# Performance work log

Hardware: AMD Instinct MI355X
Metric: run time of the kernel (lower is better)

Reference implementation:

```python
import jax, jax.numpy as jnp
import numpy as np

NUM_ITER = 3  # num_itterations

def squash(s):
    # Faithful to the module's (non-standard) squash: out = |s|^2 * s / (1 + |s|^2 * (|s| + 1e-9)).
    # torch sums over dim=-2 of [..., D, 1]; here s is [..., D] so sum over last axis.
    sq = jnp.sum(s * s, axis=-1, keepdims=True)
    norm = jnp.sqrt(sq)
    return sq * s / (1.0 + sq * (norm + 1e-9))

def setup_inputs() -> dict:
    key = jax.random.key(0)
    k1, k2 = jax.random.split(key)
    B, P, N, T, D = 512, 1152, 10, 16, 8
    x = jax.random.normal(k1, (B, P, D), dtype=jnp.float32)          # input capsules
    W = jax.random.normal(k2, (P, N, T, D), dtype=jnp.float32)       # routing transform (torch W with leading 1 dropped)
    return {"x": x, "W": W}

def reference(x, B_unused=None, *, _=None, **__):
    raise RuntimeError('placeholder')

def reference(x, W):
    # prediction u_hat[b,p,n,:] = W[p,n] @ x[b,p]  -> [B, P, N, T]
    pred = jnp.einsum('pntd,bpd->bpnt', W, x)
    B, P, N = pred.shape[0], pred.shape[1], pred.shape[2]
    b_ij = jnp.zeros((B, P, N), dtype=x.dtype)
    v = None
    for i in range(NUM_ITER):
        # torch.tensor(c_ij) detaches the coupling coefficients from the graph
        c = jax.lax.stop_gradient(jax.nn.softmax(b_ij, axis=2))      # softmax over next-caps dim
        s = jnp.einsum('bpn,bpnt->bnt', c, pred)                     # weighted sum over prev caps
        v = squash(s)                                                # [B, N, T]
        if i < NUM_ITER - 1:
            a = jnp.einsum('bpnt,bnt->bpn', pred, v)                 # agreement
            b_ij = b_ij + jnp.mean(a, axis=0, keepdims=True)         # torch mean over batch, keepdim, broadcast-add
    return v[..., None]  # [B, numNextCaps, nextCapsDim, 1] matching torch v_j.squeeze(1)
```

## Files before the change

kernel.cpp:

```cpp
#include <hip/hip_runtime.h>
#include <hip/hip_bf16.h>


typedef __attribute__((ext_vector_type(8))) short bfrag;
typedef __attribute__((ext_vector_type(4))) float f32x4;

constexpr int B_ = 512, P_ = 1152, N_ = 10, NT_ = 160;
constexpr int K1_ = 9216, NKC_ = 288;

__device__ __forceinline__ unsigned short f2bf(float f) {
    unsigned u = __float_as_uint(f);
    return (unsigned short)((u + 0x7fffu + ((u >> 16) & 1u)) >> 16);
}
__device__ __forceinline__ float bf2f(unsigned short s) {
    return __uint_as_float((unsigned)s << 16);
}
__device__ __forceinline__ bfrag mkfrag(f32x4 a, f32x4 b, float c) {
    bfrag f;
    f[0] = (short)f2bf(a.x * c); f[1] = (short)f2bf(a.y * c);
    f[2] = (short)f2bf(a.z * c); f[3] = (short)f2bf(a.w * c);
    f[4] = (short)f2bf(b.x * c); f[5] = (short)f2bf(b.y * c);
    f[6] = (short)f2bf(b.z * c); f[7] = (short)f2bf(b.w * c);
    return f;
}

__global__ __launch_bounds__(256) void k_prep(const float* __restrict__ x,
                                              const float* __restrict__ W,
                                              unsigned short* __restrict__ Xb,
                                              unsigned short* __restrict__ Xga,
                                              unsigned short* __restrict__ Wc,
                                              unsigned short* __restrict__ Wb) {
    __shared__ float smem[5760];
    const int bid = blockIdx.x, tid = threadIdx.x;
    const int w = tid >> 6, ln = tid & 63, col = ln & 15, q = ln >> 4;
    if (bid < 288) {
        const int pb = bid;
        const int p0 = pb * 4;
#pragma unroll
        for (int k = 0; k < 20; ++k) {
            const int e = k * 256 + tid;
            const int pl = e / 1280, rem = e % 1280;
            const int row = rem >> 3, d = rem & 7;
            smem[pl * 1440 + row * 9 + d] = W[(size_t)p0 * 1280 + e];
        }
        __syncthreads();
        for (int n = w; n < N_; n += 4) {
            const float* src = smem + q * 1440 + (n * 16 + col) * 9;
            bfrag f;
#pragma unroll
            for (int j = 0; j < 8; ++j) f[j] = (short)f2bf(src[j] * 0.1f);
            *(bfrag*)(Wc + ((size_t)(n * NKC_ + pb)) * 512 + ln * 8) = f;
        }
        if (tid < 128) {
            const int pdblk_l = tid >> 6;
            const int lane = tid & 63, c2 = lane & 15, q2 = lane >> 4;
            const int p_l = (pdblk_l * 16 + c2) >> 3, d = c2 & 7;
            const float* src = smem + p_l * 1440 + d;
            unsigned short* dst = Wb + ((size_t)((2 * pb + pdblk_l) * 64 + lane)) * 40;
#pragma unroll
            for (int mt = 0; mt < N_; ++mt)
#pragma unroll
                for (int r = 0; r < 4; ++r)
                    dst[mt * 4 + r] = f2bf(src[(mt * 16 + q2 * 4 + r) * 9]);
        }
    } else {
        unsigned short (*tile)[72] = (unsigned short (*)[72])smem;
        const int tb = bid - 288;
        const int pd0 = (tb >> 3) * 64, b0 = (tb & 7) * 64;
        const int c0 = tid & 63, r0 = tid >> 6;
#pragma unroll
        for (int i = 0; i < 16; ++i) {
            const int br = i * 4 + r0;
            tile[c0][br] = f2bf(x[(size_t)(b0 + br) * K1_ + pd0 + c0]);
        }
        __syncthreads();
#pragma unroll
        for (int fi = 0; fi < 2; ++fi) {
            const int f = w + fi * 4;
            const int pdblk_l = f & 3, kc_l = f >> 2;
            bfrag fr;
#pragma unroll
            for (int j = 0; j < 8; ++j)
                fr[j] = (short)tile[pdblk_l * 16 + col][kc_l * 32 + q * 8 + j];
            const size_t addr = ((size_t)(((pd0 >> 4) + pdblk_l) * 16 + (b0 >> 5) + kc_l)) * 512 + ln * 8;
            *(bfrag*)(Xga + addr) = fr;
        }
#pragma unroll
        for (int fi = 0; fi < 2; ++fi) {
            const int f = w + fi * 4;
            const int mblk_l = f & 3, kc_l = f >> 2;
            bfrag fr;
#pragma unroll
            for (int j = 0; j < 8; ++j)
                fr[j] = (short)tile[kc_l * 32 + q * 8 + j][mblk_l * 16 + col];
            const size_t addr = ((size_t)(((b0 >> 4) + mblk_l) * NKC_ + (pd0 >> 5) + kc_l)) * 512 + ln * 8;
            *(bfrag*)(Xb + addr) = fr;
        }
    }
}

__global__ __launch_bounds__(1024) void k_sv(const unsigned short* __restrict__ Xb,
                                             const unsigned short* __restrict__ Wc,
                                             unsigned short* __restrict__ Vt,
                                             float* __restrict__ outp,
                                             int final_it) {
    __shared__ float red[16][2][256];
    const int tid = threadIdx.x;
    const int w = tid >> 6, lane = tid & 63, col = lane & 15, q = lane >> 4;
    const int mblk = blockIdx.x;
    const int n0 = blockIdx.y * 2;

    f32x4 accA = (f32x4){0.f, 0.f, 0.f, 0.f};
    f32x4 accB = (f32x4){0.f, 0.f, 0.f, 0.f};
    const int kc0 = w * 18;
    const unsigned short* Xp = Xb + ((size_t)(mblk * NKC_ + kc0)) * 512 + lane * 8;
    const unsigned short* W0 = Wc + ((size_t)(n0 * NKC_ + kc0)) * 512 + lane * 8;
    const unsigned short* W1 = W0 + (size_t)NKC_ * 512;
#pragma unroll 3
    for (int i = 0; i < 18; ++i) {
        const bfrag a  = *(const bfrag*)Xp;
        const bfrag b0 = *(const bfrag*)W0;
        const bfrag b1 = *(const bfrag*)W1;
        accA = __builtin_amdgcn_mfma_f32_16x16x32_bf16(a, b0, accA, 0, 0, 0);
        accB = __builtin_amdgcn_mfma_f32_16x16x32_bf16(a, b1, accB, 0, 0, 0);
        Xp += 512; W0 += 512; W1 += 512;
    }
#pragma unroll
    for (int r = 0; r < 4; ++r) {
        red[w][0][r * 64 + q * 16 + col] = accA[r];
        red[w][1][r * 64 + q * 16 + col] = accB[r];
    }
    __syncthreads();
    if (w < 2) {
        const int mt = n0 + w;
#pragma unroll
        for (int r = 0; r < 4; ++r) {
            const int li = r * 64 + q * 16 + col;
            float s = 0.f;
#pragma unroll
            for (int j = 0; j < 16; ++j) s += red[j][w][li];
            float sq = s * s;
            sq += __shfl_xor(sq, 1);
            sq += __shfl_xor(sq, 2);
            sq += __shfl_xor(sq, 4);
            sq += __shfl_xor(sq, 8);
            const float norm = sqrtf(sq);
            const float scale = sq / (1.0f + sq * (norm + 1e-9f));
            const float vv = s * scale;
            const int b = mblk * 16 + q * 4 + r;
            if (final_it) {
                outp[(size_t)b * NT_ + mt * 16 + col] = vv;
            } else {
                const int b5 = b & 31;
                Vt[((size_t)((mblk >> 1) * N_ + mt)) * 512
                   + ((b5 >> 3) * 16 + col) * 8 + (b5 & 7)] = f2bf(vv);
            }
        }
    }
}

__global__ __launch_bounds__(768) void k_ga(const unsigned short* __restrict__ Vt,
                                            const unsigned short* __restrict__ Xga,
                                            const unsigned short* __restrict__ Wb,
                                            const float* __restrict__ W,
                                            float* __restrict__ bbar,
                                            unsigned short* __restrict__ Wc,
                                            int accum) {
    __shared__ float bred[3][3][64][41];
    __shared__ float csm[6][N_];
    const int tid = threadIdx.x;
    const int w = tid >> 6, lane = tid & 63, col = lane & 15, q = lane >> 4;
    const int third = w >> 2, wl = w & 3;
    const int pdblk = blockIdx.x * 3 + third;
    const int p = (pdblk * 16 + col) >> 3, d = col & 7;

    f32x4 acc[N_];
#pragma unroll
    for (int mt = 0; mt < N_; ++mt) acc[mt] = (f32x4){0.f, 0.f, 0.f, 0.f};

    const int kb0 = wl * 4;
#pragma unroll
    for (int kc = kb0; kc < kb0 + 4; ++kc) {
        const bfrag bf = *(const bfrag*)(Xga + ((size_t)(pdblk * 16 + kc)) * 512 + lane * 8);
#pragma unroll
        for (int mt = 0; mt < N_; ++mt) {
            const bfrag af = *(const bfrag*)(Vt + ((size_t)(kc * N_ + mt)) * 512 + lane * 8);
            acc[mt] = __builtin_amdgcn_mfma_f32_16x16x32_bf16(af, bf, acc[mt], 0, 0, 0);
        }
    }
    if (wl) {
#pragma unroll
        for (int mt = 0; mt < N_; ++mt)
#pragma unroll
            for (int r = 0; r < 4; ++r)
                bred[third][wl - 1][lane][mt * 4 + r] = acc[mt][r];
    }
    __syncthreads();
    if (wl == 0) {
        unsigned short wv[40];
        const unsigned short* ws2 = Wb + ((size_t)(pdblk * 64 + lane)) * 40;
#pragma unroll
        for (int v = 0; v < 40; ++v) wv[v] = ws2[v];
        float part[N_];
#pragma unroll
        for (int mt = 0; mt < N_; ++mt) {
            float s = 0.f;
#pragma unroll
            for (int r = 0; r < 4; ++r) {
                const float h = acc[mt][r] + bred[third][0][lane][mt * 4 + r]
                              + bred[third][1][lane][mt * 4 + r]
                              + bred[third][2][lane][mt * 4 + r];
                s = fmaf(bf2f(wv[mt * 4 + r]), h, s);
            }
            s += __shfl_xor(s, 1);
            s += __shfl_xor(s, 2);
            s += __shfl_xor(s, 4);
            s += __shfl_xor(s, 16);
            s += __shfl_xor(s, 32);
            part[mt] = s;
        }
        if (q == 0 && d == 0) {
            const int pl = col >> 3;
            float bv[N_];
#pragma unroll
            for (int mt = 0; mt < N_; ++mt) {
                bv[mt] = part[mt] * (1.0f / 512.0f);
                if (accum) bv[mt] += bbar[(size_t)p * N_ + mt];
                bbar[(size_t)p * N_ + mt] = bv[mt];
            }
            float m = -1e30f;
#pragma unroll
            for (int mt = 0; mt < N_; ++mt) m = fmaxf(m, bv[mt]);
            float sum = 0.f;
#pragma unroll
            for (int mt = 0; mt < N_; ++mt) { bv[mt] = __expf(bv[mt] - m); sum += bv[mt]; }
            const float inv = 1.f / sum;
#pragma unroll
            for (int mt = 0; mt < N_; ++mt) csm[third * 2 + pl][mt] = bv[mt] * inv;
        }
    }
    __syncthreads();
    const int p0 = blockIdx.x * 6;
#pragma unroll
    for (int task = tid; task < 960; task += 768) {
        const int pl = task / 160, rem = task % 160;
        const int n = rem >> 4, cl = rem & 15;
        const int pp = p0 + pl;
        const float c = csm[pl][n];
        const float* wr = W + ((size_t)pp * NT_ + n * 16 + cl) * 8;
        const size_t addr = ((size_t)(n * NKC_ + (pp >> 2))) * 512 + (pp & 3) * 128 + cl * 8;
        *(bfrag*)(Wc + addr) = mkfrag(*(const f32x4*)wr, *(const f32x4*)(wr + 4), c);
    }
}

extern "C" void kernel_launch(void* const* d_in, const int* in_sizes, int n_in,
                              void* d_out, int out_size, void* d_ws, size_t ws_size,
                              hipStream_t stream) {
    const float* x = (const float*)d_in[0];
    const float* W = (const float*)d_in[1];

    char* wsp = (char*)d_ws;
    float* bbar = (float*)wsp;
    unsigned short* Xb  = (unsigned short*)(wsp + 46080);
    unsigned short* Xga = Xb + (size_t)32 * NKC_ * 512;
    unsigned short* Wc  = Xga + (size_t)576 * 16 * 512;
    unsigned short* Wb  = Wc + (size_t)N_ * NKC_ * 512;
    unsigned short* Vt  = Wb + (size_t)576 * 64 * 40;
    float* outp = (float*)d_out;

    k_prep<<<dim3(1440), dim3(256), 0, stream>>>(x, W, Xb, Xga, Wc, Wb);
    k_sv<<<dim3(32, 5), dim3(1024), 0, stream>>>(Xb, Wc, Vt, outp, 0);
    k_ga<<<dim3(192), dim3(768), 0, stream>>>(Vt, Xga, Wb, W, bbar, Wc, 0);
    k_sv<<<dim3(32, 5), dim3(1024), 0, stream>>>(Xb, Wc, Vt, outp, 0);
    k_ga<<<dim3(192), dim3(768), 0, stream>>>(Vt, Xga, Wb, W, bbar, Wc, 1);
    k_sv<<<dim3(32, 5), dim3(1024), 0, stream>>>(Xb, Wc, Vt, outp, 1);
}
```

Measured before the change: 133.4 us.

## Apply coupling coefficients to X fragments in k_sv instead of rewriting scaled W

k_ga now only writes the per-capsule softmax coefficients to a small global buffer, instead of re-reading fp32 W and rewriting the bf16 coefficient-scaled W tensor. k_prep writes an unscaled bf16 copy of W alongside the uniform 0.1-scaled copy used in the first pass. Later k_sv passes scale the X fragments by the coefficients on the fly before each MFMA. This removes a large W read and write per routing iteration, but adds per-element convert and multiply work in the k_sv inner loop and one extra W copy in the prep kernel.

```diff
diff --git a/kernel.cpp b/kernel.cpp
--- a/kernel.cpp
+++ b/kernel.cpp
@@ -14,21 +14,14 @@
 }
 __device__ __forceinline__ float bf2f(unsigned short s) {
     return __uint_as_float((unsigned)s << 16);
-}
-__device__ __forceinline__ bfrag mkfrag(f32x4 a, f32x4 b, float c) {
-    bfrag f;
-    f[0] = (short)f2bf(a.x * c); f[1] = (short)f2bf(a.y * c);
-    f[2] = (short)f2bf(a.z * c); f[3] = (short)f2bf(a.w * c);
-    f[4] = (short)f2bf(b.x * c); f[5] = (short)f2bf(b.y * c);
-    f[6] = (short)f2bf(b.z * c); f[7] = (short)f2bf(b.w * c);
-    return f;
 }
 
 __global__ __launch_bounds__(256) void k_prep(const float* __restrict__ x,
                                               const float* __restrict__ W,
                                               unsigned short* __restrict__ Xb,
                                               unsigned short* __restrict__ Xga,
-                                              unsigned short* __restrict__ Wc,
+                                              unsigned short* __restrict__ Wc0,
+                                              unsigned short* __restrict__ Wst,
                                               unsigned short* __restrict__ Wb) {
     __shared__ float smem[5760];
     const int bid = blockIdx.x, tid = threadIdx.x;
@@ -46,10 +39,16 @@
         __syncthreads();
         for (int n = w; n < N_; n += 4) {
             const float* src = smem + q * 1440 + (n * 16 + col) * 9;
-            bfrag f;
-#pragma unroll
-            for (int j = 0; j < 8; ++j) f[j] = (short)f2bf(src[j] * 0.1f);
-            *(bfrag*)(Wc + ((size_t)(n * NKC_ + pb)) * 512 + ln * 8) = f;
+            bfrag f0, f1;
+#pragma unroll
+            for (int j = 0; j < 8; ++j) {
+                const float v = src[j];
+                f0[j] = (short)f2bf(v * 0.1f);
+                f1[j] = (short)f2bf(v);
+            }
+            const size_t addr = ((size_t)(n * NKC_ + pb)) * 512 + ln * 8;
+            *(bfrag*)(Wc0 + addr) = f0;
+            *(bfrag*)(Wst + addr) = f1;
         }
         if (tid < 128) {
             const int pdblk_l = tid >> 6;
@@ -100,10 +99,11 @@
 }
 
 __global__ __launch_bounds__(1024) void k_sv(const unsigned short* __restrict__ Xb,
-                                             const unsigned short* __restrict__ Wc,
+                                             const unsigned short* __restrict__ Wf,
+                                             const float* __restrict__ csm,
                                              unsigned short* __restrict__ Vt,
                                              float* __restrict__ outp,
-                                             int final_it) {
+                                             int mode) {
     __shared__ float red[16][2][256];
     const int tid = threadIdx.x;
     const int w = tid >> 6, lane = tid & 63, col = lane & 15, q = lane >> 4;
@@ -114,16 +114,37 @@
     f32x4 accB = (f32x4){0.f, 0.f, 0.f, 0.f};
     const int kc0 = w * 18;
     const unsigned short* Xp = Xb + ((size_t)(mblk * NKC_ + kc0)) * 512 + lane * 8;
-    const unsigned short* W0 = Wc + ((size_t)(n0 * NKC_ + kc0)) * 512 + lane * 8;
+    const unsigned short* W0 = Wf + ((size_t)(n0 * NKC_ + kc0)) * 512 + lane * 8;
     const unsigned short* W1 = W0 + (size_t)NKC_ * 512;
+    if (mode == 0) {
 #pragma unroll 3
-    for (int i = 0; i < 18; ++i) {
-        const bfrag a  = *(const bfrag*)Xp;
-        const bfrag b0 = *(const bfrag*)W0;
-        const bfrag b1 = *(const bfrag*)W1;
-        accA = __builtin_amdgcn_mfma_f32_16x16x32_bf16(a, b0, accA, 0, 0, 0);
-        accB = __builtin_amdgcn_mfma_f32_16x16x32_bf16(a, b1, accB, 0, 0, 0);
-        Xp += 512; W0 += 512; W1 += 512;
+        for (int i = 0; i < 18; ++i) {
+            const bfrag a  = *(const bfrag*)Xp;
+            const bfrag b0 = *(const bfrag*)W0;
+            const bfrag b1 = *(const bfrag*)W1;
+            accA = __builtin_amdgcn_mfma_f32_16x16x32_bf16(a, b0, accA, 0, 0, 0);
+            accB = __builtin_amdgcn_mfma_f32_16x16x32_bf16(a, b1, accB, 0, 0, 0);
+            Xp += 512; W0 += 512; W1 += 512;
+        }
+    } else {
+        const float* cp = csm + ((size_t)(kc0 * 4 + q)) * N_ + n0;
+#pragma unroll 3
+        for (int i = 0; i < 18; ++i) {
+            const bfrag a  = *(const bfrag*)Xp;
+            const bfrag b0 = *(const bfrag*)W0;
+            const bfrag b1 = *(const bfrag*)W1;
+            const float2 cc = *(const float2*)cp;
+            bfrag a0, a1;
+#pragma unroll
+            for (int j = 0; j < 8; ++j) {
+                const float xf = bf2f((unsigned short)a[j]);
+                a0[j] = (short)f2bf(xf * cc.x);
+                a1[j] = (short)f2bf(xf * cc.y);
+            }
+            accA = __builtin_amdgcn_mfma_f32_16x16x32_bf16(a0, b0, accA, 0, 0, 0);
+            accB = __builtin_amdgcn_mfma_f32_16x16x32_bf16(a1, b1, accB, 0, 0, 0);
+            Xp += 512; W0 += 512; W1 += 512; cp += 40;
+        }
     }
 #pragma unroll
     for (int r = 0; r < 4; ++r) {
@@ -148,7 +169,7 @@
             const float scale = sq / (1.0f + sq * (norm + 1e-9f));
             const float vv = s * scale;
             const int b = mblk * 16 + q * 4 + r;
-            if (final_it) {
+            if (mode == 2) {
                 outp[(size_t)b * NT_ + mt * 16 + col] = vv;
             } else {
                 const int b5 = b & 31;
@@ -162,12 +183,10 @@
 __global__ __launch_bounds__(768) void k_ga(const unsigned short* __restrict__ Vt,
                                             const unsigned short* __restrict__ Xga,
                                             const unsigned short* __restrict__ Wb,
-                                            const float* __restrict__ W,
                                             float* __restrict__ bbar,
-                                            unsigned short* __restrict__ Wc,
+                                            float* __restrict__ csm_g,
                                             int accum) {
     __shared__ float bred[3][3][64][41];
-    __shared__ float csm[6][N_];
     const int tid = threadIdx.x;
     const int w = tid >> 6, lane = tid & 63, col = lane & 15, q = lane >> 4;
     const int third = w >> 2, wl = w & 3;
@@ -220,7 +239,6 @@
             part[mt] = s;
         }
         if (q == 0 && d == 0) {
-            const int pl = col >> 3;
             float bv[N_];
 #pragma unroll
             for (int mt = 0; mt < N_; ++mt) {
@@ -236,20 +254,9 @@
             for (int mt = 0; mt < N_; ++mt) { bv[mt] = __expf(bv[mt] - m); sum += bv[mt]; }
             const float inv = 1.f / sum;
 #pragma unroll
-            for (int mt = 0; mt < N_; ++mt) csm[third * 2 + pl][mt] = bv[mt] * inv;
-        }
-    }
-    __syncthreads();
-    const int p0 = blockIdx.x * 6;
-#pragma unroll
-    for (int task = tid; task < 960; task += 768) {
-        const int pl = task / 160, rem = task % 160;
-        const int n = rem >> 4, cl = rem & 15;
-        const int pp = p0 + pl;
-        const float c = csm[pl][n];
-        const float* wr = W + ((size_t)pp * NT_ + n * 16 + cl) * 8;
-        const size_t addr = ((size_t)(n * NKC_ + (pp >> 2))) * 512 + (pp & 3) * 128 + cl * 8;
-        *(bfrag*)(Wc + addr) = mkfrag(*(const f32x4*)wr, *(const f32x4*)(wr + 4), c);
+            for (int mt = 0; mt < N_; ++mt)
+                csm_g[(size_t)p * N_ + mt] = bv[mt] * inv;
+        }
     }
 }
 
@@ -261,17 +268,19 @@
 
     char* wsp = (char*)d_ws;
     float* bbar = (float*)wsp;
-    unsigned short* Xb  = (unsigned short*)(wsp + 46080);
+    float* csm  = (float*)(wsp + 46080);
+    unsigned short* Xb  = (unsigned short*)(wsp + 92160);
     unsigned short* Xga = Xb + (size_t)32 * NKC_ * 512;
-    unsigned short* Wc  = Xga + (size_t)576 * 16 * 512;
-    unsigned short* Wb  = Wc + (size_t)N_ * NKC_ * 512;
+    unsigned short* Wc0 = Xga + (size_t)576 * 16 * 512;
+    unsigned short* Wst = Wc0 + (size_t)N_ * NKC_ * 512;
+    unsigned short* Wb  = Wst + (size_t)N_ * NKC_ * 512;
     unsigned short* Vt  = Wb + (size_t)576 * 64 * 40;
     float* outp = (float*)d_out;
 
-    k_prep<<<dim3(1440), dim3(256), 0, stream>>>(x, W, Xb, Xga, Wc, Wb);
-    k_sv<<<dim3(32, 5), dim3(1024), 0, stream>>>(Xb, Wc, Vt, outp, 0);
-    k_ga<<<dim3(192), dim3(768), 0, stream>>>(Vt, Xga, Wb, W, bbar, Wc, 0);
-    k_sv<<<dim3(32, 5), dim3(1024), 0, stream>>>(Xb, Wc, Vt, outp, 0);
-    k_ga<<<dim3(192), dim3(768), 0, stream>>>(Vt, Xga, Wb, W, bbar, Wc, 1);
-    k_sv<<<dim3(32, 5), dim3(1024), 0, stream>>>(Xb, Wc, Vt, outp, 1);
-}
+    k_prep<<<dim3(1440), dim3(256), 0, stream>>>(x, W, Xb, Xga, Wc0, Wst, Wb);
+    k_sv<<<dim3(32, 5), dim3(1024), 0, stream>>>(Xb, Wc0, csm, Vt, outp, 0);
+    k_ga<<<dim3(192), dim3(768), 0, stream>>>(Vt, Xga, Wb, bbar, csm, 0);
+    k_sv<<<dim3(32, 5), dim3(1024), 0, stream>>>(Xb, Wst, csm, Vt, outp, 1);
+    k_ga<<<dim3(192), dim3(768), 0, stream>>>(Vt, Xga, Wb, bbar, csm, 1);
+    k_sv<<<dim3(32, 5), dim3(1024), 0, stream>>>(Xb, Wst, csm, Vt, outp, 2);
+}
```

After: 136.3 us. 1.02x slower.

## Restructure agreement kernel to split N across waves with LDS double-buffered staging

Applied to the files above, without the earlier changes.

The agreement kernel previously had each wave compute all 10 next-capsule tiles over a quarter of the batch chunks, then reduce partials through a large shared-memory buffer. Now each block covers 2 pd-blocks with 10 waves, each wave owning 2 next-capsule tiles over the full batch. V and X fragments are staged cooperatively into a double-buffered LDS tile, with the next chunk prefetched into registers. The Wb weights are repacked into 8-wide vector fragments so each wave does a single vector load. This removes the cross-wave reduction and cuts register pressure, and the grid grows from 192 to 288 blocks, at the cost of two barriers per k-step.

```diff
diff --git a/kernel.cpp b/kernel.cpp
--- a/kernel.cpp
+++ b/kernel.cpp
@@ -29,7 +29,7 @@
                                               unsigned short* __restrict__ Xb,
                                               unsigned short* __restrict__ Xga,
                                               unsigned short* __restrict__ Wc,
-                                              unsigned short* __restrict__ Wb) {
+                                              unsigned short* __restrict__ Wb2) {
     __shared__ float smem[5760];
     const int bid = blockIdx.x, tid = threadIdx.x;
     const int w = tid >> 6, ln = tid & 63, col = ln & 15, q = ln >> 4;
@@ -56,12 +56,16 @@
             const int lane = tid & 63, c2 = lane & 15, q2 = lane >> 4;
             const int p_l = (pdblk_l * 16 + c2) >> 3, d = c2 & 7;
             const float* src = smem + p_l * 1440 + d;
-            unsigned short* dst = Wb + ((size_t)((2 * pb + pdblk_l) * 64 + lane)) * 40;
-#pragma unroll
-            for (int mt = 0; mt < N_; ++mt)
-#pragma unroll
-                for (int r = 0; r < 4; ++r)
-                    dst[mt * 4 + r] = f2bf(src[(mt * 16 + q2 * 4 + r) * 9]);
+#pragma unroll
+            for (int mtg = 0; mtg < 5; ++mtg) {
+                bfrag f;
+#pragma unroll
+                for (int ml = 0; ml < 2; ++ml)
+#pragma unroll
+                    for (int r = 0; r < 4; ++r)
+                        f[ml * 4 + r] = (short)f2bf(src[((mtg * 2 + ml) * 16 + q2 * 4 + r) * 9]);
+                *(bfrag*)(Wb2 + ((size_t)((2 * pb + pdblk_l) * 5 + mtg) * 64 + lane) * 8) = f;
+            }
         }
     } else {
         unsigned short (*tile)[72] = (unsigned short (*)[72])smem;
@@ -159,94 +163,105 @@
     }
 }
 
-__global__ __launch_bounds__(768) void k_ga(const unsigned short* __restrict__ Vt,
+__global__ __launch_bounds__(640) void k_ga(const unsigned short* __restrict__ Vt,
                                             const unsigned short* __restrict__ Xga,
-                                            const unsigned short* __restrict__ Wb,
+                                            const unsigned short* __restrict__ Wb2,
                                             const float* __restrict__ W,
                                             float* __restrict__ bbar,
                                             unsigned short* __restrict__ Wc,
                                             int accum) {
-    __shared__ float bred[3][3][64][41];
-    __shared__ float csm[6][N_];
+    __shared__ unsigned short stage[2][6144];
+    __shared__ float csm_part[2][2][N_];
+    __shared__ float csm_l[4][N_];
     const int tid = threadIdx.x;
-    const int w = tid >> 6, lane = tid & 63, col = lane & 15, q = lane >> 4;
-    const int third = w >> 2, wl = w & 3;
-    const int pdblk = blockIdx.x * 3 + third;
-    const int p = (pdblk * 16 + col) >> 3, d = col & 7;
-
-    f32x4 acc[N_];
-#pragma unroll
-    for (int mt = 0; mt < N_; ++mt) acc[mt] = (f32x4){0.f, 0.f, 0.f, 0.f};
-
-    const int kb0 = wl * 4;
-#pragma unroll
-    for (int kc = kb0; kc < kb0 + 4; ++kc) {
-        const bfrag bf = *(const bfrag*)(Xga + ((size_t)(pdblk * 16 + kc)) * 512 + lane * 8);
+    const int w = tid >> 6, ln = tid & 63, col = ln & 15, q = ln >> 4;
+    const int pdh = w / 5, mtg = w % 5;
+    const int bx = blockIdx.x;
+    const int pdblk = bx * 2 + pdh;
+    const int mt0 = mtg * 2;
+
+    const unsigned short* vsrc0 = Vt + (size_t)(tid >> 6) * 512 + (tid & 63) * 8;
+    const unsigned short* xsrc0 = (tid < 128)
+        ? Xga + ((size_t)((bx * 2 + (tid >> 6)) * 16)) * 512 + (tid & 63) * 8
+        : nullptr;
+
+    bfrag pa = *(const bfrag*)vsrc0;
+    bfrag pb;
+    if (tid < 128) pb = *(const bfrag*)xsrc0;
+    *(bfrag*)(&stage[0][tid * 8]) = pa;
+    if (tid < 128) *(bfrag*)(&stage[0][(640 + tid) * 8]) = pb;
+    __syncthreads();
+
+    f32x4 acc0 = (f32x4){0.f, 0.f, 0.f, 0.f};
+    f32x4 acc1 = (f32x4){0.f, 0.f, 0.f, 0.f};
+    for (int kc = 0; kc < 16; ++kc) {
+        if (kc < 15) {
+            pa = *(const bfrag*)(vsrc0 + (size_t)(kc + 1) * N_ * 512);
+            if (tid < 128) pb = *(const bfrag*)(xsrc0 + (size_t)(kc + 1) * 512);
+        }
+        const unsigned short* sb = stage[kc & 1];
+        const bfrag bf  = *(const bfrag*)(sb + (640 + pdh * 64 + ln) * 8);
+        const bfrag af0 = *(const bfrag*)(sb + (mt0 * 64 + ln) * 8);
+        const bfrag af1 = *(const bfrag*)(sb + ((mt0 + 1) * 64 + ln) * 8);
+        acc0 = __builtin_amdgcn_mfma_f32_16x16x32_bf16(af0, bf, acc0, 0, 0, 0);
+        acc1 = __builtin_amdgcn_mfma_f32_16x16x32_bf16(af1, bf, acc1, 0, 0, 0);
+        if (kc < 15) {
+            __syncthreads();
+            unsigned short* db = stage[(kc + 1) & 1];
+            *(bfrag*)(&db[tid * 8]) = pa;
+            if (tid < 128) *(bfrag*)(&db[(640 + tid) * 8]) = pb;
+            __syncthreads();
+        }
+    }
+
+    const bfrag wv = *(const bfrag*)(Wb2 + ((size_t)(pdblk * 5 + mtg) * 64 + ln) * 8);
+    float part[2];
+#pragma unroll
+    for (int ml = 0; ml < 2; ++ml) {
+        const f32x4 a = ml ? acc1 : acc0;
+        float s = 0.f;
+#pragma unroll
+        for (int r = 0; r < 4; ++r)
+            s = fmaf(bf2f((unsigned short)wv[ml * 4 + r]), a[r], s);
+        s += __shfl_xor(s, 1);
+        s += __shfl_xor(s, 2);
+        s += __shfl_xor(s, 4);
+        s += __shfl_xor(s, 16);
+        s += __shfl_xor(s, 32);
+        part[ml] = s;
+    }
+    if (q == 0 && (col & 7) == 0) {
+        const int pl = col >> 3;
+        csm_part[pdh][pl][mt0] = part[0];
+        csm_part[pdh][pl][mt0 + 1] = part[1];
+    }
+    __syncthreads();
+    if (tid < 4) {
+        const int ph = tid >> 1, pl = tid & 1;
+        const int p = bx * 4 + ph * 2 + pl;
+        float bv[N_];
 #pragma unroll
         for (int mt = 0; mt < N_; ++mt) {
-            const bfrag af = *(const bfrag*)(Vt + ((size_t)(kc * N_ + mt)) * 512 + lane * 8);
-            acc[mt] = __builtin_amdgcn_mfma_f32_16x16x32_bf16(af, bf, acc[mt], 0, 0, 0);
-        }
-    }
-    if (wl) {
-#pragma unroll
-        for (int mt = 0; mt < N_; ++mt)
-#pragma unroll
-            for (int r = 0; r < 4; ++r)
-                bred[third][wl - 1][lane][mt * 4 + r] = acc[mt][r];
-    }
-    __syncthreads();
-    if (wl == 0) {
-        unsigned short wv[40];
-        const unsigned short* ws2 = Wb + ((size_t)(pdblk * 64 + lane)) * 40;
-#pragma unroll
-        for (int v = 0; v < 40; ++v) wv[v] = ws2[v];
-        float part[N_];
-#pragma unroll
-        for (int mt = 0; mt < N_; ++mt) {
-            float s = 0.f;
-#pragma unroll
-            for (int r = 0; r < 4; ++r) {
-                const float h = acc[mt][r] + bred[third][0][lane][mt * 4 + r]
-                              + bred[third][1][lane][mt * 4 + r]
-                              + bred[third][2][lane][mt * 4 + r];
-                s = fmaf(bf2f(wv[mt * 4 + r]), h, s);
-            }
-            s += __shfl_xor(s, 1);
-            s += __shfl_xor(s, 2);
-            s += __shfl_xor(s, 4);
-            s += __shfl_xor(s, 16);
-            s += __shfl_xor(s, 32);
-            part[mt] = s;
-        }
-        if (q == 0 && d == 0) {
-            const int pl = col >> 3;
-            float bv[N_];
-#pragma unroll
-            for (int mt = 0; mt < N_; ++mt) {
-                bv[mt] = part[mt] * (1.0f / 512.0f);
-                if (accum) bv[mt] += bbar[(size_t)p * N_ + mt];
-                bbar[(size_t)p * N_ + mt] = bv[mt];
-            }
-            float m = -1e30f;
-#pragma unroll
-            for (int mt = 0; mt < N_; ++mt) m = fmaxf(m, bv[mt]);
-            float sum = 0.f;
-#pragma unroll
-            for (int mt = 0; mt < N_; ++mt) { bv[mt] = __expf(bv[mt] - m); sum += bv[mt]; }
-            const float inv = 1.f / sum;
-#pragma unroll
-            for (int mt = 0; mt < N_; ++mt) csm[third * 2 + pl][mt] = bv[mt] * inv;
-        }
-    }
-    __syncthreads();
-    const int p0 = blockIdx.x * 6;
-#pragma unroll
-    for (int task = tid; task < 960; task += 768) {
-        const int pl = task / 160, rem = task % 160;
+            bv[mt] = csm_part[ph][pl][mt] * (1.0f / 512.0f);
+            if (accum) bv[mt] += bbar[(size_t)p * N_ + mt];
+            bbar[(size_t)p * N_ + mt] = bv[mt];
+        }
+        float m = -1e30f;
+#pragma unroll
+        for (int mt = 0; mt < N_; ++mt) m = fmaxf(m, bv[mt]);
+        float sum = 0.f;
+#pragma unroll
+        for (int mt = 0; mt < N_; ++mt) { bv[mt] = __expf(bv[mt] - m); sum += bv[mt]; }
+        const float inv = 1.f / sum;
+#pragma unroll
+        for (int mt = 0; mt < N_; ++mt) csm_l[tid][mt] = bv[mt] * inv;
+    }
+    __syncthreads();
+    {
+        const int pl4 = tid / 160, rem = tid % 160;
         const int n = rem >> 4, cl = rem & 15;
-        const int pp = p0 + pl;
-        const float c = csm[pl][n];
+        const int pp = bx * 4 + pl4;
+        const float c = csm_l[pl4][n];
         const float* wr = W + ((size_t)pp * NT_ + n * 16 + cl) * 8;
         const size_t addr = ((size_t)(n * NKC_ + (pp >> 2))) * 512 + (pp & 3) * 128 + cl * 8;
         *(bfrag*)(Wc + addr) = mkfrag(*(const f32x4*)wr, *(const f32x4*)(wr + 4), c);
@@ -264,14 +279,14 @@
     unsigned short* Xb  = (unsigned short*)(wsp + 46080);
     unsigned short* Xga = Xb + (size_t)32 * NKC_ * 512;
     unsigned short* Wc  = Xga + (size_t)576 * 16 * 512;
-    unsigned short* Wb  = Wc + (size_t)N_ * NKC_ * 512;
-    unsigned short* Vt  = Wb + (size_t)576 * 64 * 40;
+    unsigned short* Wb2 = Wc + (size_t)N_ * NKC_ * 512;
+    unsigned short* Vt  = Wb2 + (size_t)576 * 5 * 64 * 8;
     float* outp = (float*)d_out;
 
-    k_prep<<<dim3(1440), dim3(256), 0, stream>>>(x, W, Xb, Xga, Wc, Wb);
+    k_prep<<<dim3(1440), dim3(256), 0, stream>>>(x, W, Xb, Xga, Wc, Wb2);
     k_sv<<<dim3(32, 5), dim3(1024), 0, stream>>>(Xb, Wc, Vt, outp, 0);
-    k_ga<<<dim3(192), dim3(768), 0, stream>>>(Vt, Xga, Wb, W, bbar, Wc, 0);
+    k_ga<<<dim3(288), dim3(640), 0, stream>>>(Vt, Xga, Wb2, W, bbar, Wc, 0);
     k_sv<<<dim3(32, 5), dim3(1024), 0, stream>>>(Xb, Wc, Vt, outp, 0);
-    k_ga<<<dim3(192), dim3(768), 0, stream>>>(Vt, Xga, Wb, W, bbar, Wc, 1);
+    k_ga<<<dim3(288), dim3(640), 0, stream>>>(Vt, Xga, Wb2, W, bbar, Wc, 1);
     k_sv<<<dim3(32, 5), dim3(1024), 0, stream>>>(Xb, Wc, Vt, outp, 1);
 }
```

After: 134.2 us. No clear change (+0.6%).
